# Optimization experiments

Hardware: AMD Instinct MI355X
Metric: run time of the kernel (lower is better)

## Reference

```python
import jax, jax.numpy as jnp
import numpy as np

B, NS, NF, D, K, N = 8192, 16, 16, 128, 32, 50000
A_H = 32          # alpha MLP hidden dim
EPS = 0.05        # entropic regularization
GW_ITER = 1
SK_ITER = 2


def setup_inputs() -> dict:
    key = jax.random.key(0)
    ks = jax.random.split(key, 10)
    adj = jax.random.uniform(ks[0], (B, NS, NS), dtype=jnp.float32)
    features = jax.random.uniform(ks[1], (N, D), dtype=jnp.float32)
    idxs = jax.random.randint(ks[2], (B, NS), 0, N + 1)  # N is the zero-pad row
    C_up = jax.random.uniform(ks[3], (NF * (NF - 1) // 2, K), minval=-1.0, maxval=1.0)
    F_filter = jax.random.uniform(ks[4], (NF, D, K))
    h_logits = 0.1 * jax.random.normal(ks[5], (NF,))
    w1 = jax.random.normal(ks[6], (D, A_H)) / np.float32(np.sqrt(D))
    b1 = jnp.zeros((A_H,), jnp.float32)
    w2 = jax.random.normal(ks[7], (A_H, 1)) / np.float32(np.sqrt(A_H))
    b2 = jnp.zeros((1,), jnp.float32)
    return dict(adj=adj, features=features, idxs=idxs, C_up=C_up, F_filter=F_filter,
                h_logits=h_logits, w1=w1, b1=b1, w2=w2, b2=b2)


def _log_sinkhorn(cost, logp, logq):
    # cost: [B,K,Ns,Nf]; logp: [B,Ns]; logq: [Nf]. Stable log-domain Sinkhorn.
    f = jnp.zeros(cost.shape[:3], cost.dtype)              # [B,K,Ns]
    g = jnp.zeros(cost.shape[:2] + cost.shape[3:], cost.dtype)  # [B,K,Nf]
    lp = logp[:, None, :]
    lq = logq[None, None, :]
    for _ in range(SK_ITER):
        f = EPS * (lp - jax.nn.logsumexp((g[:, :, None, :] - cost) / EPS, axis=3))
        g = EPS * (lq - jax.nn.logsumexp((f[:, :, :, None] - cost) / EPS, axis=2))
    return jnp.exp((f[..., None] + g[:, :, None, :] - cost) / EPS)  # transport plan


def reference(adj, features, idxs, C_up, F_filter, h_logits, w1, b1, w2, b2):
    nf, d, k = F_filter.shape
    # symmetric filter adjacency from upper-triangle params (ReLU'd)
    iu, ju = jnp.triu_indices(nf, 1)
    C = jnp.zeros((nf, nf, k), C_up.dtype).at[iu, ju].set(jax.nn.relu(C_up))
    C = C + jnp.swapaxes(C, 0, 1)                          # [Nf,Nf,K]

    # gather subgraph features (zero pad row at index N)
    x = jnp.concatenate([features, jnp.zeros((1, d), features.dtype)], axis=0)
    x = x[idxs]                                            # [B,Ns,D]
    b, ns, _ = x.shape

    h_sub = jnp.full((b, ns), 1.0 / ns, x.dtype)           # uniform subgraph weights
    h_fil = jax.nn.softmax(h_logits)                       # [Nf]

    # local alpha gate from pooled subgraph features
    pooled = x.mean(axis=1)                                # [B,D]
    alpha = jax.nn.sigmoid(jax.nn.relu(pooled @ w1 + b1) @ w2 + b2)  # [B,1]
    alpha = alpha[:, :, None, None]                        # [B,1,1,1]

    # feature cost M[b,k,i,j] = ||x_bi - F_filter[j,:,k]||^2
    x2 = jnp.sum(x * x, -1)                                # [B,Ns]
    f2 = jnp.sum(F_filter * F_filter, 1)                   # [Nf,K]
    xf = jnp.einsum('bid,jdk->bkij', x, F_filter)          # [B,K,Ns,Nf]
    M = x2[:, None, :, None] + f2.T[None, :, None, :] - 2.0 * xf

    # GW square-loss constants
    constC1 = jnp.einsum('bip,bp->bi', adj * adj, h_sub)   # [B,Ns]
    constC2 = jnp.einsum('pjk,p->jk', C * C, h_fil)        # [Nf,K]

    def gw_tens(T):
        cross = jnp.einsum('bip,bkpq,qjk->bkij', adj, T, C)  # [B,K,Ns,Nf]
        return constC1[:, None, :, None] + constC2.T[None, :, None, :] - 2.0 * cross

    # init plan: outer(h_sub, h_fil), shared across K
    T = jnp.broadcast_to((h_sub[:, :, None] * h_fil[None, None, :])[:, None],
                         (b, k, ns, nf))
    logp = jnp.log(h_sub)
    logq = jnp.log(h_fil)
    for _ in range(GW_ITER):
        cost = (1.0 - alpha) * M + alpha * gw_tens(T)
        T = _log_sinkhorn(cost, logp, logq)
    final_cost = (1.0 - alpha) * M + alpha * gw_tens(T)
    fgw_dists = jnp.sum(T * final_cost, axis=(2, 3))       # [B,K]
    return fgw_dists
```

## Files before the change

### kernel.cpp

```cpp
#include <hip/hip_runtime.h>

typedef unsigned short ushort;
typedef unsigned int uint;
typedef __attribute__((ext_vector_type(8))) short short8;
typedef __attribute__((ext_vector_type(4))) float f32x4;

#define B_    8192
#define D_    128
#define K_    32
#define NV_   50000
#define SC_   28.853900817779268f
#define ISC_  0.03465735902799726f

#define WS_HF    0
#define WS_LHF2  16
#define WS_CCT   32
#define WS_CC2T  544
#define WS_F2    1056
#define WS_W1T   1568
#define WSB_FBHI 22656
#define WSB_FBLO 153728
#define WSB_CB1  284800

__device__ __forceinline__ ushort bf16rne(float v) {
    uint u = __float_as_uint(v);
    uint r = (u + 0x7fffu + ((u >> 16) & 1u)) >> 16;
    return (ushort)r;
}
__device__ __forceinline__ float bf16tof(ushort h) { return __uint_as_float(((uint)h) << 16); }

template <int C>
__device__ __forceinline__ float dppmv(float x) {
    return __int_as_float(__builtin_amdgcn_update_dpp(
        __float_as_int(x), __float_as_int(x), C, 0xf, 0xf, false));
}
__device__ __forceinline__ float rowmax16(float x) {
    x = fmaxf(x, dppmv<0x121>(x));
    x = fmaxf(x, dppmv<0x122>(x));
    x = fmaxf(x, dppmv<0x124>(x));
    x = fmaxf(x, dppmv<0x128>(x));
    return x;
}
__device__ __forceinline__ float rowsum16(float x) {
    x += dppmv<0x121>(x);
    x += dppmv<0x122>(x);
    x += dppmv<0x124>(x);
    x += dppmv<0x128>(x);
    return x;
}
__device__ __forceinline__ f32x4 mfma16(short8 a, short8 b, f32x4 c) {
    return __builtin_amdgcn_mfma_f32_16x16x32_bf16(a, b, c, 0, 0, 0);
}
__device__ __forceinline__ uint cvtpk_bf16(float a, float b) {
    uint r;
    asm("v_cvt_pk_bf16_f32 %0, %1, %2" : "=v"(r) : "v"(a), "v"(b));
    return r;
}

__global__ __launch_bounds__(512) void init_fb(const float* __restrict__ Ff, float* __restrict__ ws) {
    int idx = blockIdx.x * 512 + threadIdx.x;
    int e = idx & 7, l = (idx >> 3) & 63, s = (idx >> 9) & 3, k = idx >> 11;
    int j = l & 15, kg = l >> 4;
    int d = s * 32 + kg * 8 + e;
    float v = Ff[(j * D_ + d) * K_ + k];
    ushort hb = bf16rne(v);
    ushort lb = bf16rne(v - bf16tof(hb));
    ushort* FBHI = (ushort*)((char*)ws + WSB_FBHI);
    ushort* FBLO = (ushort*)((char*)ws + WSB_FBLO);
    FBHI[idx] = hb;
    FBLO[idx] = lb;
}

__global__ __launch_bounds__(1024) void init_small(
    const float* __restrict__ C_up, const float* __restrict__ Ff,
    const float* __restrict__ h_logits, const float* __restrict__ w1,
    float* __restrict__ ws) {
    __shared__ float hf[16];
    __shared__ float Cs[16][16][32];
    __shared__ float f2p[16][32][2];
    const int t = threadIdx.x;

    if (t == 0) {
        float m = -3.4e38f;
        for (int p = 0; p < 16; ++p) m = fmaxf(m, h_logits[p]);
        float e[16], s = 0.f;
        for (int p = 0; p < 16; ++p) { e[p] = __expf(h_logits[p] - m); s += e[p]; }
        for (int p = 0; p < 16; ++p) {
            hf[p] = e[p] / s;
            ws[WS_HF + p] = hf[p];
            ws[WS_LHF2 + p] = log2f(hf[p]);
        }
    }
    for (int e0 = t; e0 < 16 * 16 * 32; e0 += 1024) {
        int k = e0 & 31, j = (e0 >> 5) & 15, q = e0 >> 9;
        float v = 0.f;
        if (q < j)      { int pi = q * (31 - q) / 2 + (j - q - 1); v = fmaxf(C_up[pi * 32 + k], 0.f); }
        else if (j < q) { int pi = j * (31 - j) / 2 + (q - j - 1); v = fmaxf(C_up[pi * 32 + k], 0.f); }
        Cs[q][j][k] = v;
    }
    for (int e0 = t; e0 < 4096; e0 += 1024) {
        int u = e0 >> 7, d = e0 & 127;
        ws[WS_W1T + e0] = w1[d * 32 + u];
    }
    __syncthreads();

    if (t < 512) {
        int k = t >> 4, j = t & 15;
        float s1 = 0.f, s2 = 0.f;
        for (int q = 0; q < 16; ++q) {
            float c = Cs[q][j][k];
            s1 += hf[q] * c;
            s2 += hf[q] * c * c;
        }
        ws[WS_CCT + k * 16 + j] = s1;
        ws[WS_CC2T + k * 16 + j] = s2;
    }
    {
        int k = t & 31, half = (t >> 5) & 1, j = t >> 6;
        float s = 0.f;
        for (int dd = 0; dd < 64; ++dd) {
            int d = half * 64 + dd;
            float f = Ff[(j * D_ + d) * K_ + k];
            s += f * f;
        }
        f2p[j][k][half] = s;
    }
    {
        ushort* CB1 = (ushort*)((char*)ws + WSB_CB1);
        for (int i0 = t; i0 < 16384; i0 += 1024) {
            int e = i0 & 7, l = (i0 >> 3) & 63, k = i0 >> 9;
            int kg = l >> 4, j = l & 15, q = (kg & 1) * 8 + e;
            CB1[i0] = (kg < 2) ? bf16rne(Cs[q][j][k]) : (ushort)0;
        }
    }
    __syncthreads();
    if (t < 512) {
        int j = t >> 5, k = t & 31;
        ws[WS_F2 + j * 32 + k] = f2p[j][k][0] + f2p[j][k][1];
    }
}

__global__ __launch_bounds__(256, 4) void fgw_main(
    const float* __restrict__ adj, const float* __restrict__ features,
    const int* __restrict__ idxs,
    const float* __restrict__ b1,
    const float* __restrict__ w2, const float* __restrict__ b2,
    const float* __restrict__ ws, float* __restrict__ out) {
    __shared__ __align__(16) ushort xA[2][4][64][8];
    __shared__ __align__(16) uint  exchbuf[2112];
    __shared__ __align__(16) ushort adjA[64][8];
    __shared__ float cct_s[512];
    __shared__ float cc2_s[512];
    __shared__ float f2_s[16][33];
    __shared__ float lhf_s[16];
    __shared__ float adj_s[16][17];
    __shared__ float pooled[128];
    __shared__ float x2part[16][8];
    __shared__ __align__(16) float x2s[16];
    __shared__ __align__(16) float c1s[16];
    __shared__ __align__(16) float rss[16];
    __shared__ float alpha_sh;
    __shared__ int idx_sh[16];

    const int t = threadIdx.x;
    const int blk = blockIdx.x;
    float* xT = (float*)exchbuf;

    #pragma unroll
    for (int e = t; e < 512; e += 256) {
        cct_s[e] = ws[WS_CCT + e];
        cc2_s[e] = ws[WS_CC2T + e];
        f2_s[e >> 5][e & 31] = ws[WS_F2 + e];
    }
    adj_s[t >> 4 & 15][t & 15] = adj[blk * 256 + (t & 255)];
    if (t < 16) {
        lhf_s[t] = ws[WS_LHF2 + t];
        idx_sh[t] = idxs[blk * 16 + t];
    }
    __syncthreads();

    if (t < 128) {
        int i = t >> 3, c = t & 7;
        int ix = idx_sh[i];
        float vv[16];
        if (ix < NV_) {
            const float4* fp = (const float4*)(features + (size_t)ix * D_ + c * 16);
            float4 q0 = fp[0], q1 = fp[1], q2 = fp[2], q3 = fp[3];
            vv[0] = q0.x; vv[1] = q0.y; vv[2] = q0.z; vv[3] = q0.w;
            vv[4] = q1.x; vv[5] = q1.y; vv[6] = q1.z; vv[7] = q1.w;
            vv[8] = q2.x; vv[9] = q2.y; vv[10] = q2.z; vv[11] = q2.w;
            vv[12] = q3.x; vv[13] = q3.y; vv[14] = q3.z; vv[15] = q3.w;
        } else {
            #pragma unroll
            for (int e = 0; e < 16; ++e) vv[e] = 0.f;
        }
        float* xrow = xT + i * 132 + c * 16;
        float s2 = 0.f;
        #pragma unroll
        for (int e = 0; e < 16; ++e) { xrow[e] = vv[e]; s2 += vv[e] * vv[e]; }
        x2part[i][c] = s2;
        #pragma unroll
        for (int g = 0; g < 2; ++g) {
            int d0 = c * 16 + g * 8;
            int s = d0 >> 5, kg = (d0 >> 3) & 3;
            union { short8 v; ushort u[8]; } h8, l8;
            #pragma unroll
            for (int e = 0; e < 8; ++e) {
                float x = vv[g * 8 + e];
                ushort hb = bf16rne(x);
                h8.u[e] = hb;
                l8.u[e] = bf16rne(x - bf16tof(hb));
            }
            *(short8*)&xA[0][s][kg * 16 + i][0] = h8.v;
            *(short8*)&xA[1][s][kg * 16 + i][0] = l8.v;
        }
    } else if (t < 192) {
        int l = t - 128;
        int i = l & 15, kg = l >> 4;
        union { short8 v; ushort u[8]; } f8;
        #pragma unroll
        for (int e = 0; e < 8; ++e) {
            int p = (kg & 1) * 8 + e;
            float v = adj_s[i][p];
            ushort hb = bf16rne(v);
            f8.u[e] = (kg < 2) ? hb : bf16rne(v - bf16tof(hb));
        }
        *(short8*)&adjA[l][0] = f8.v;
    } else if (t < 208) {
        int i = t - 192;
        float s = 0.f, s2 = 0.f;
        for (int p = 0; p < 16; ++p) { float a = adj_s[i][p]; s += a; s2 += a * a; }
        rss[i] = s * (1.f / 16.f);
        c1s[i] = s2 * (1.f / 16.f);
    }
    __syncthreads();

    if (t < 128) {
        int d = t;
        float s = 0.f;
        for (int i = 0; i < 16; ++i) s += xT[i * 132 + d];
        pooled[d] = s * (1.f / 16.f);
    } else if (t < 144) {
        int i = t - 128;
        float s = 0.f;
        #pragma unroll
        for (int c = 0; c < 8; ++c) s += x2part[i][c];
        x2s[i] = s;
    }
    __syncthreads();

    if (t < 32) {
        int u = t;
        float h = b1[u];
        const float4* wrow = (const float4*)(ws + WS_W1T + u * 128);
        #pragma unroll 4
        for (int dd = 0; dd < 32; ++dd) {
            float4 w4 = wrow[dd];
            h = fmaf(pooled[dd * 4 + 0], w4.x, h);
            h = fmaf(pooled[dd * 4 + 1], w4.y, h);
            h = fmaf(pooled[dd * 4 + 2], w4.z, h);
            h = fmaf(pooled[dd * 4 + 3], w4.w, h);
        }
        h = fmaxf(h, 0.f);
        float z = h * w2[u];
        #pragma unroll
        for (int s = 1; s < 32; s <<= 1) z += __shfl_xor(z, s);
        if (u == 0) alpha_sh = 1.f / (1.f + __expf(-(z + b2[0])));
    }
    __syncthreads();

    const int w = t >> 6, l = t & 63;
    const int jl = l & 15, ig = l >> 4;
    const float lq2 = lhf_s[jl];
    const ushort* FBHI = (const ushort*)((const char*)ws + WSB_FBHI);
    const ushort* FBLO = (const ushort*)((const char*)ws + WSB_FBLO);
    const ushort* CB1  = (const ushort*)((const char*)ws + WSB_CB1);
    uint* Tb = exchbuf + w * 384;
    uint* Mb = Tb + 192;

    const float alpha = alpha_sh, oma = 1.f - alpha;
    const short8 Aadj = *(const short8*)&adjA[l][0];
    const f32x4 x2v = *(const f32x4*)&x2s[ig * 4];
    const f32x4 c1v = *(const f32x4*)&c1s[ig * 4];
    const f32x4 rsv = *(const f32x4*)&rss[ig * 4];

    #pragma unroll 1
    for (int kk = 0; kk < 8; ++kk) {
        const int k = kk * 4 + w;
        f32x4 acc = {0.f, 0.f, 0.f, 0.f};
        #pragma unroll
        for (int s = 0; s < 4; ++s) {
            const short8 Bh = *(const short8*)(FBHI + ((k * 4 + s) * 64 + l) * 8);
            const short8 Bl = *(const short8*)(FBLO + ((k * 4 + s) * 64 + l) * 8);
            const short8 Ah = *(const short8*)&xA[0][s][l][0];
            const short8 Al = *(const short8*)&xA[1][s][l][0];
            acc = mfma16(Ah, Bh, acc);
            acc = mfma16(Al, Bh, acc);
            acc = mfma16(Ah, Bl, acc);
        }
        const float f2v  = f2_s[jl][k];
        const float cctv = cct_s[k * 16 + jl];
        const float cc2v = cc2_s[k * 16 + jl];
        const short8 C1f = *(const short8*)(CB1 + (k * 64 + l) * 8);

        float Chat[4], rc[4];
        #pragma unroll
        for (int r = 0; r < 4; ++r) {
            float M = x2v[r] + f2v - 2.f * acc[r];
            rc[r] = rsv[r] * cctv;
            float gw0 = c1v[r] + cc2v - 2.f * rc[r];
            Chat[r] = SC_ * (oma * M + alpha * gw0);
        }
        float G = 0.f, Fh[4];
        #pragma unroll
        for (int it = 0; it < 2; ++it) {
            #pragma unroll
            for (int r = 0; r < 4; ++r) {
                float a = G - Chat[r];
                float m = rowmax16(a);
                float e = exp2f(a - m);
                float S = rowsum16(e);
                Fh[r] = -4.f - m - log2f(S);
            }
            float diff[4];
            #pragma unroll
            for (int r = 0; r < 4; ++r) diff[r] = Fh[r] - Chat[r];
            float m2 = fmaxf(fmaxf(diff[0], diff[1]), fmaxf(diff[2], diff[3]));
            m2 = fmaxf(m2, __shfl_xor(m2, 16));
            m2 = fmaxf(m2, __shfl_xor(m2, 32));
            float S2 = 0.f;
            #pragma unroll
            for (int r = 0; r < 4; ++r) S2 += exp2f(diff[r] - m2);
            S2 += __shfl_xor(S2, 16);
            S2 += __shfl_xor(S2, 32);
            G = lq2 - m2 - log2f(S2);
        }
        float Tv[4];
        #pragma unroll
        for (int r = 0; r < 4; ++r) Tv[r] = exp2f(Fh[r] + G - Chat[r]);

        Tb[jl * 12 + ig * 2]     = cvtpk_bf16(Tv[0], Tv[1]);
        Tb[jl * 12 + ig * 2 + 1] = cvtpk_bf16(Tv[2], Tv[3]);
        const short8 Bt = *(const short8*)&Tb[jl * 12 + (ig & 1) * 4];
        f32x4 tmpv = mfma16(Aadj, Bt, (f32x4){0.f, 0.f, 0.f, 0.f});

        ushort* Mbs = (ushort*)Mb;
        #pragma unroll
        for (int r = 0; r < 4; ++r)
            Mbs[(ig * 4 + r) * 24 + jl] = bf16rne(tmpv[r]);
        const short8 Atm = *(const short8*)&Mbs[jl * 24 + (ig & 1) * 8];
        f32x4 cr = mfma16(Atm, C1f, (f32x4){0.f, 0.f, 0.f, 0.f});

        float dot = 0.f;
        #pragma unroll
        for (int r = 0; r < 4; ++r) {
            float fc = Chat[r] * ISC_ + 2.f * alpha * (rc[r] - cr[r]);
            dot = fmaf(Tv[r], fc, dot);
        }
        dot = rowsum16(dot);
        dot += __shfl_xor(dot, 16);
        dot += __shfl_xor(dot, 32);
        if (l == 0) out[blk * K_ + k] = dot;
    }
}

extern "C" void kernel_launch(void* const* d_in, const int* in_sizes, int n_in,
                              void* d_out, int out_size, void* d_ws, size_t ws_size,
                              hipStream_t stream) {
    (void)in_sizes; (void)n_in; (void)out_size; (void)ws_size;
    const float* adj      = (const float*)d_in[0];
    const float* features = (const float*)d_in[1];
    const int*   idxs     = (const int*)  d_in[2];
    const float* C_up     = (const float*)d_in[3];
    const float* Ff       = (const float*)d_in[4];
    const float* h_logits = (const float*)d_in[5];
    const float* w1       = (const float*)d_in[6];
    const float* b1       = (const float*)d_in[7];
    const float* w2       = (const float*)d_in[8];
    const float* b2       = (const float*)d_in[9];
    float* out = (float*)d_out;
    float* ws  = (float*)d_ws;

    hipLaunchKernelGGL(init_fb, dim3(128), dim3(512), 0, stream, Ff, ws);
    hipLaunchKernelGGL(init_small, dim3(1), dim3(1024), 0, stream, C_up, Ff, h_logits, w1, ws);
    hipLaunchKernelGGL(fgw_main, dim3(B_), dim3(256), 0, stream,
                       adj, features, idxs, b1, w2, b2, ws, out);
}
```

Measured before the change: 289.1 us.

## Split alpha MLP into own kernel, pack per-k tables, simplify Sinkhorn first iteration

Moves the mean-pool and alpha MLP out of the main kernel into a separate per-graph kernel that writes alpha to the workspace. The per-k constants (cct, cc2, f2) are packed into one float4 table read straight from global memory instead of staged in LDS. The first Sinkhorn iteration uses a row min because G is zero there, and the final plan reuses the last column exponentials instead of recomputing exp. The smaller LDS footprint allows a higher launch-bounds occupancy (6 blocks per CU), at the cost of an extra launch and re-reading the gathered features a second time.

```diff
diff --git a/kernel.cpp b/kernel.cpp
--- a/kernel.cpp
+++ b/kernel.cpp
@@ -14,13 +14,12 @@
 
 #define WS_HF    0
 #define WS_LHF2  16
-#define WS_CCT   32
-#define WS_CC2T  544
-#define WS_F2    1056
-#define WS_W1T   1568
-#define WSB_FBHI 22656
-#define WSB_FBLO 153728
-#define WSB_CB1  284800
+#define WS_W1T   32
+#define WS_TBL   4128
+#define WS_ALPHA 6176
+#define WSB_FBHI 57472
+#define WSB_FBLO 188544
+#define WSB_CB1  319616
 
 __device__ __forceinline__ ushort bf16rne(float v) {
     uint u = __float_as_uint(v);
@@ -39,6 +38,13 @@
     x = fmaxf(x, dppmv<0x122>(x));
     x = fmaxf(x, dppmv<0x124>(x));
     x = fmaxf(x, dppmv<0x128>(x));
+    return x;
+}
+__device__ __forceinline__ float rowmin16(float x) {
+    x = fminf(x, dppmv<0x121>(x));
+    x = fminf(x, dppmv<0x122>(x));
+    x = fminf(x, dppmv<0x124>(x));
+    x = fminf(x, dppmv<0x128>(x));
     return x;
 }
 __device__ __forceinline__ float rowsum16(float x) {
@@ -102,6 +108,16 @@
         int u = e0 >> 7, d = e0 & 127;
         ws[WS_W1T + e0] = w1[d * 32 + u];
     }
+    {
+        int k = t & 31, half = (t >> 5) & 1, j = t >> 6;
+        float s = 0.f;
+        for (int dd = 0; dd < 64; ++dd) {
+            int d = half * 64 + dd;
+            float f = Ff[(j * D_ + d) * K_ + k];
+            s += f * f;
+        }
+        f2p[j][k][half] = s;
+    }
     __syncthreads();
 
     if (t < 512) {
@@ -112,18 +128,13 @@
             s1 += hf[q] * c;
             s2 += hf[q] * c * c;
         }
-        ws[WS_CCT + k * 16 + j] = s1;
-        ws[WS_CC2T + k * 16 + j] = s2;
-    }
-    {
-        int k = t & 31, half = (t >> 5) & 1, j = t >> 6;
-        float s = 0.f;
-        for (int dd = 0; dd < 64; ++dd) {
-            int d = half * 64 + dd;
-            float f = Ff[(j * D_ + d) * K_ + k];
-            s += f * f;
-        }
-        f2p[j][k][half] = s;
+        ws[WS_TBL + t * 4 + 0] = s1;
+        ws[WS_TBL + t * 4 + 1] = s2;
+        ws[WS_TBL + t * 4 + 3] = 0.f;
+    } else {
+        int t2 = t - 512;
+        int j = t2 >> 5, k = t2 & 31;
+        ws[WS_TBL + (k * 16 + j) * 4 + 2] = f2p[j][k][0] + f2p[j][k][1];
     }
     {
         ushort* CB1 = (ushort*)((char*)ws + WSB_CB1);
@@ -133,50 +144,68 @@
             CB1[i0] = (kg < 2) ? bf16rne(Cs[q][j][k]) : (ushort)0;
         }
     }
-    __syncthreads();
-    if (t < 512) {
-        int j = t >> 5, k = t & 31;
-        ws[WS_F2 + j * 32 + k] = f2p[j][k][0] + f2p[j][k][1];
-    }
-}
-
-__global__ __launch_bounds__(256, 4) void fgw_main(
+}
+
+__global__ __launch_bounds__(64) void alpha_k(
+    const float* __restrict__ features, const int* __restrict__ idxs,
+    const float* __restrict__ b1, const float* __restrict__ w2,
+    const float* __restrict__ b2, float* __restrict__ ws) {
+    __shared__ float pooled_s[128];
+    __shared__ int idl[16];
+    const int b = blockIdx.x, l = threadIdx.x;
+    if (l < 16) idl[l] = idxs[b * 16 + l];
+    __syncthreads();
+    float p0 = 0.f, p1 = 0.f;
+    #pragma unroll 4
+    for (int i = 0; i < 16; ++i) {
+        int ix = idl[i];
+        if (ix < NV_) {
+            p0 += features[(size_t)ix * D_ + l];
+            p1 += features[(size_t)ix * D_ + 64 + l];
+        }
+    }
+    pooled_s[l] = p0 * (1.f / 16.f);
+    pooled_s[64 + l] = p1 * (1.f / 16.f);
+    __syncthreads();
+    float z = 0.f;
+    if (l < 32) {
+        float h = b1[l];
+        const float4* wrow = (const float4*)(ws + WS_W1T + l * 128);
+        #pragma unroll 4
+        for (int dd = 0; dd < 32; ++dd) {
+            float4 w4 = wrow[dd];
+            h = fmaf(pooled_s[dd * 4 + 0], w4.x, h);
+            h = fmaf(pooled_s[dd * 4 + 1], w4.y, h);
+            h = fmaf(pooled_s[dd * 4 + 2], w4.z, h);
+            h = fmaf(pooled_s[dd * 4 + 3], w4.w, h);
+        }
+        h = fmaxf(h, 0.f);
+        z = h * w2[l];
+    }
+    #pragma unroll
+    for (int s = 1; s < 64; s <<= 1) z += __shfl_xor(z, s);
+    if (l == 0) ws[WS_ALPHA + b] = 1.f / (1.f + __expf(-(z + b2[0])));
+}
+
+__global__ __launch_bounds__(256, 6) void fgw_main(
     const float* __restrict__ adj, const float* __restrict__ features,
     const int* __restrict__ idxs,
-    const float* __restrict__ b1,
-    const float* __restrict__ w2, const float* __restrict__ b2,
     const float* __restrict__ ws, float* __restrict__ out) {
     __shared__ __align__(16) ushort xA[2][4][64][8];
-    __shared__ __align__(16) uint  exchbuf[2112];
+    __shared__ __align__(16) uint  exchbuf[1536];
     __shared__ __align__(16) ushort adjA[64][8];
-    __shared__ float cct_s[512];
-    __shared__ float cc2_s[512];
-    __shared__ float f2_s[16][33];
-    __shared__ float lhf_s[16];
     __shared__ float adj_s[16][17];
-    __shared__ float pooled[128];
     __shared__ float x2part[16][8];
     __shared__ __align__(16) float x2s[16];
     __shared__ __align__(16) float c1s[16];
     __shared__ __align__(16) float rss[16];
-    __shared__ float alpha_sh;
     __shared__ int idx_sh[16];
 
     const int t = threadIdx.x;
     const int blk = blockIdx.x;
-    float* xT = (float*)exchbuf;
-
-    #pragma unroll
-    for (int e = t; e < 512; e += 256) {
-        cct_s[e] = ws[WS_CCT + e];
-        cc2_s[e] = ws[WS_CC2T + e];
-        f2_s[e >> 5][e & 31] = ws[WS_F2 + e];
-    }
-    adj_s[t >> 4 & 15][t & 15] = adj[blk * 256 + (t & 255)];
-    if (t < 16) {
-        lhf_s[t] = ws[WS_LHF2 + t];
-        idx_sh[t] = idxs[blk * 16 + t];
-    }
+
+    adj_s[(t >> 4) & 15][t & 15] = adj[blk * 256 + t];
+    if (t < 16) idx_sh[t] = idxs[blk * 16 + t];
     __syncthreads();
 
     if (t < 128) {
@@ -194,10 +223,9 @@
             #pragma unroll
             for (int e = 0; e < 16; ++e) vv[e] = 0.f;
         }
-        float* xrow = xT + i * 132 + c * 16;
         float s2 = 0.f;
         #pragma unroll
-        for (int e = 0; e < 16; ++e) { xrow[e] = vv[e]; s2 += vv[e] * vv[e]; }
+        for (int e = 0; e < 16; ++e) s2 += vv[e] * vv[e];
         x2part[i][c] = s2;
         #pragma unroll
         for (int g = 0; g < 2; ++g) {
@@ -234,133 +262,131 @@
         c1s[i] = s2 * (1.f / 16.f);
     }
     __syncthreads();
-
-    if (t < 128) {
-        int d = t;
+    if (t < 16) {
         float s = 0.f;
-        for (int i = 0; i < 16; ++i) s += xT[i * 132 + d];
-        pooled[d] = s * (1.f / 16.f);
-    } else if (t < 144) {
-        int i = t - 128;
-        float s = 0.f;
-        #pragma unroll
-        for (int c = 0; c < 8; ++c) s += x2part[i][c];
-        x2s[i] = s;
-    }
-    __syncthreads();
-
-    if (t < 32) {
-        int u = t;
-        float h = b1[u];
-        const float4* wrow = (const float4*)(ws + WS_W1T + u * 128);
-        #pragma unroll 4
-        for (int dd = 0; dd < 32; ++dd) {
-            float4 w4 = wrow[dd];
-            h = fmaf(pooled[dd * 4 + 0], w4.x, h);
-            h = fmaf(pooled[dd * 4 + 1], w4.y, h);
-            h = fmaf(pooled[dd * 4 + 2], w4.z, h);
-            h = fmaf(pooled[dd * 4 + 3], w4.w, h);
-        }
-        h = fmaxf(h, 0.f);
-        float z = h * w2[u];
-        #pragma unroll
-        for (int s = 1; s < 32; s <<= 1) z += __shfl_xor(z, s);
-        if (u == 0) alpha_sh = 1.f / (1.f + __expf(-(z + b2[0])));
+        #pragma unroll
+        for (int c = 0; c < 8; ++c) s += x2part[t][c];
+        x2s[t] = s;
     }
     __syncthreads();
 
     const int w = t >> 6, l = t & 63;
     const int jl = l & 15, ig = l >> 4;
-    const float lq2 = lhf_s[jl];
-    const ushort* FBHI = (const ushort*)((const char*)ws + WSB_FBHI);
-    const ushort* FBLO = (const ushort*)((const char*)ws + WSB_FBLO);
-    const ushort* CB1  = (const ushort*)((const char*)ws + WSB_CB1);
-    uint* Tb = exchbuf + w * 384;
-    uint* Mb = Tb + 192;
-
-    const float alpha = alpha_sh, oma = 1.f - alpha;
+
+    const float alpha = ws[WS_ALPHA + blk];
+    const float oma = 1.f - alpha;
+    const float soma = SC_ * oma, salpha = SC_ * alpha, ta2 = 2.f * alpha;
+    const float n2soma = -2.f * soma;
+    const float lq2 = ws[WS_LHF2 + jl];
+    const float hfj = ws[WS_HF + jl];
     const short8 Aadj = *(const short8*)&adjA[l][0];
     const f32x4 x2v = *(const f32x4*)&x2s[ig * 4];
     const f32x4 c1v = *(const f32x4*)&c1s[ig * 4];
     const f32x4 rsv = *(const f32x4*)&rss[ig * 4];
+    float A1[4], mB1[4], TB1[4];
+    #pragma unroll
+    for (int r = 0; r < 4; ++r) {
+        A1[r]  = fmaf(soma, x2v[r], salpha * c1v[r]);
+        mB1[r] = -2.f * salpha * rsv[r];
+        TB1[r] = ta2 * rsv[r];
+    }
+
+    const char* pH = (const char*)ws + WSB_FBHI + (w * 4) * 1024 + l * 16;
+    const char* pL = (const char*)ws + WSB_FBLO + (w * 4) * 1024 + l * 16;
+    const char* pC = (const char*)ws + WSB_CB1 + w * 1024 + l * 16;
+    const float* pT = ws + WS_TBL + (w * 16 + jl) * 4;
+    uint* Tb = exchbuf + w * 384;
+    ushort* Mbs = (ushort*)(Tb + 192);
 
     #pragma unroll 1
     for (int kk = 0; kk < 8; ++kk) {
-        const int k = kk * 4 + w;
         f32x4 acc = {0.f, 0.f, 0.f, 0.f};
         #pragma unroll
         for (int s = 0; s < 4; ++s) {
-            const short8 Bh = *(const short8*)(FBHI + ((k * 4 + s) * 64 + l) * 8);
-            const short8 Bl = *(const short8*)(FBLO + ((k * 4 + s) * 64 + l) * 8);
+            const short8 Bh = *(const short8*)(pH + s * 1024);
+            const short8 Bl = *(const short8*)(pL + s * 1024);
             const short8 Ah = *(const short8*)&xA[0][s][l][0];
             const short8 Al = *(const short8*)&xA[1][s][l][0];
             acc = mfma16(Ah, Bh, acc);
             acc = mfma16(Al, Bh, acc);
             acc = mfma16(Ah, Bl, acc);
         }
-        const float f2v  = f2_s[jl][k];
-        const float cctv = cct_s[k * 16 + jl];
-        const float cc2v = cc2_s[k * 16 + jl];
-        const short8 C1f = *(const short8*)(CB1 + (k * 64 + l) * 8);
-
-        float Chat[4], rc[4];
+        pH += 16384; pL += 16384;
+        const short8 C1f = *(const short8*)pC; pC += 4096;
+        const float4 tb = *(const float4*)pT; pT += 256;
+        const float cctv = tb.x, cc2v = tb.y, f2v = tb.z;
+
+        const float c0 = fmaf(soma, f2v, salpha * cc2v);
+        float Chat[4];
+        #pragma unroll
+        for (int r = 0; r < 4; ++r)
+            Chat[r] = fmaf(n2soma, acc[r], fmaf(mB1[r], cctv, A1[r] + c0));
+
+        float Fh[4];
         #pragma unroll
         for (int r = 0; r < 4; ++r) {
-            float M = x2v[r] + f2v - 2.f * acc[r];
-            rc[r] = rsv[r] * cctv;
-            float gw0 = c1v[r] + cc2v - 2.f * rc[r];
-            Chat[r] = SC_ * (oma * M + alpha * gw0);
-        }
-        float G = 0.f, Fh[4];
-        #pragma unroll
-        for (int it = 0; it < 2; ++it) {
-            #pragma unroll
-            for (int r = 0; r < 4; ++r) {
-                float a = G - Chat[r];
-                float m = rowmax16(a);
-                float e = exp2f(a - m);
-                float S = rowsum16(e);
-                Fh[r] = -4.f - m - log2f(S);
-            }
-            float diff[4];
-            #pragma unroll
-            for (int r = 0; r < 4; ++r) diff[r] = Fh[r] - Chat[r];
-            float m2 = fmaxf(fmaxf(diff[0], diff[1]), fmaxf(diff[2], diff[3]));
-            m2 = fmaxf(m2, __shfl_xor(m2, 16));
-            m2 = fmaxf(m2, __shfl_xor(m2, 32));
-            float S2 = 0.f;
-            #pragma unroll
-            for (int r = 0; r < 4; ++r) S2 += exp2f(diff[r] - m2);
-            S2 += __shfl_xor(S2, 16);
-            S2 += __shfl_xor(S2, 32);
-            G = lq2 - m2 - log2f(S2);
-        }
+            float mn = rowmin16(Chat[r]);
+            float e = exp2f(mn - Chat[r]);
+            float S = rowsum16(e);
+            Fh[r] = (mn - 4.f) - log2f(S);
+        }
+        float diff[4];
+        #pragma unroll
+        for (int r = 0; r < 4; ++r) diff[r] = Fh[r] - Chat[r];
+        float m2 = fmaxf(fmaxf(fmaxf(diff[0], diff[1]), diff[2]), diff[3]);
+        m2 = fmaxf(m2, __shfl_xor(m2, 16));
+        m2 = fmaxf(m2, __shfl_xor(m2, 32));
+        float S2 = 0.f;
+        #pragma unroll
+        for (int r = 0; r < 4; ++r) S2 += exp2f(diff[r] - m2);
+        S2 += __shfl_xor(S2, 16);
+        S2 += __shfl_xor(S2, 32);
+        float G = lq2 - m2 - log2f(S2);
+        #pragma unroll
+        for (int r = 0; r < 4; ++r) {
+            float a = G - Chat[r];
+            float m = rowmax16(a);
+            float e = exp2f(a - m);
+            float S = rowsum16(e);
+            Fh[r] = (-4.f - m) - log2f(S);
+        }
+        #pragma unroll
+        for (int r = 0; r < 4; ++r) diff[r] = Fh[r] - Chat[r];
+        m2 = fmaxf(fmaxf(fmaxf(diff[0], diff[1]), diff[2]), diff[3]);
+        m2 = fmaxf(m2, __shfl_xor(m2, 16));
+        m2 = fmaxf(m2, __shfl_xor(m2, 32));
+        float e2[4];
+        S2 = 0.f;
+        #pragma unroll
+        for (int r = 0; r < 4; ++r) { e2[r] = exp2f(diff[r] - m2); S2 += e2[r]; }
+        S2 += __shfl_xor(S2, 16);
+        S2 += __shfl_xor(S2, 32);
+        const float wgt = hfj * __builtin_amdgcn_rcpf(S2);
         float Tv[4];
         #pragma unroll
-        for (int r = 0; r < 4; ++r) Tv[r] = exp2f(Fh[r] + G - Chat[r]);
+        for (int r = 0; r < 4; ++r) Tv[r] = e2[r] * wgt;
 
         Tb[jl * 12 + ig * 2]     = cvtpk_bf16(Tv[0], Tv[1]);
         Tb[jl * 12 + ig * 2 + 1] = cvtpk_bf16(Tv[2], Tv[3]);
         const short8 Bt = *(const short8*)&Tb[jl * 12 + (ig & 1) * 4];
         f32x4 tmpv = mfma16(Aadj, Bt, (f32x4){0.f, 0.f, 0.f, 0.f});
 
-        ushort* Mbs = (ushort*)Mb;
         #pragma unroll
         for (int r = 0; r < 4; ++r)
-            Mbs[(ig * 4 + r) * 24 + jl] = bf16rne(tmpv[r]);
+            Mbs[(ig * 4 + r) * 24 + jl] = (ushort)cvtpk_bf16(tmpv[r], tmpv[r]);
         const short8 Atm = *(const short8*)&Mbs[jl * 24 + (ig & 1) * 8];
         f32x4 cr = mfma16(Atm, C1f, (f32x4){0.f, 0.f, 0.f, 0.f});
 
         float dot = 0.f;
         #pragma unroll
         for (int r = 0; r < 4; ++r) {
-            float fc = Chat[r] * ISC_ + 2.f * alpha * (rc[r] - cr[r]);
+            float fc = fmaf(ISC_, Chat[r], fmaf(TB1[r], cctv, -ta2 * cr[r]));
             dot = fmaf(Tv[r], fc, dot);
         }
         dot = rowsum16(dot);
         dot += __shfl_xor(dot, 16);
         dot += __shfl_xor(dot, 32);
-        if (l == 0) out[blk * K_ + k] = dot;
+        if (l == 0) out[blk * K_ + kk * 4 + w] = dot;
     }
 }
 
@@ -383,6 +409,7 @@
 
     hipLaunchKernelGGL(init_fb, dim3(128), dim3(512), 0, stream, Ff, ws);
     hipLaunchKernelGGL(init_small, dim3(1), dim3(1024), 0, stream, C_up, Ff, h_logits, w1, ws);
+    hipLaunchKernelGGL(alpha_k, dim3(B_), dim3(64), 0, stream, features, idxs, b1, w2, b2, ws);
     hipLaunchKernelGGL(fgw_main, dim3(B_), dim3(256), 0, stream,
-                       adj, features, idxs, b1, w2, b2, ws, out);
-}
+                       adj, features, idxs, ws, out);
+}
```

Result: slower. 297.6 us, median of 2 (+2.9%).
